# Kernel tuning notes

Measured on AMD Instinct MI355X. Metric: run time of the kernel, lower is better.

## Reference

```python
import jax, jax.numpy as jnp
import numpy as np

DIM = 2048
N_HEADS = 16
HEAD_DIM = DIM // N_HEADS
EPS = 1e-6


def setup_inputs() -> dict:
    key = jax.random.key(0)
    k1, k2, k3, k4, k5 = jax.random.split(key, 5)
    B, S = 2, 2048
    x = jax.random.normal(k1, (B, S, DIM), dtype=jnp.float32)
    cos = jax.random.uniform(k2, (S, HEAD_DIM), dtype=jnp.float32)
    sin = jax.random.uniform(k3, (S, HEAD_DIM), dtype=jnp.float32)
    # torch nn.Linear convention: weight [out_features, in_features], y = x @ W.T
    W_qkv = jax.random.normal(k4, (3 * DIM, DIM), dtype=jnp.float32) * 0.02
    W_proj = jax.random.normal(k5, (DIM, DIM), dtype=jnp.float32) * 0.02
    return {"x": x, "cos": cos, "sin": sin, "W_qkv": W_qkv, "W_proj": W_proj}


def _apply_rope(x, cos, sin):
    # x: [B,H,S,D], cos/sin: [S,D]; rotate interleaved even/odd pairs
    x1, x2 = x[..., ::2], x[..., 1::2]
    c = cos[:, ::2][None, None]  # [1,1,S,D/2]
    s = sin[:, ::2][None, None]
    y1 = x1 * c - x2 * s
    y2 = x1 * s + x2 * c
    return jnp.stack([y1, y2], axis=-1).reshape(x.shape)


def _rms_norm(x):
    # per-head RMS normalization over last dim, no learned scale
    return x * jax.lax.rsqrt(jnp.mean(x * x, axis=-1, keepdims=True) + EPS)


def reference(x, cos, sin, W_qkv, W_proj):
    b, s, d = x.shape
    qkv = jnp.einsum('bsd,ed->bse', x, W_qkv)  # [B,S,3*dim]
    q, k, v = jnp.split(qkv, 3, axis=-1)
    # [B,S,dim] -> [B,H,S,Dh]
    def to_heads(t):
        return t.reshape(b, s, N_HEADS, HEAD_DIM).transpose(0, 2, 1, 3)
    q, k, v = to_heads(q), to_heads(k), to_heads(v)
    q = _apply_rope(_rms_norm(q), cos, sin)
    k = _apply_rope(_rms_norm(k), cos, sin)
    scale = 1.0 / jnp.sqrt(jnp.asarray(HEAD_DIM, dtype=x.dtype))
    scores = jnp.einsum('bhqd,bhkd->bhqk', q, k) * scale  # [B,H,S,S]
    attn = jax.nn.softmax(scores, axis=-1)
    out = jnp.einsum('bhqk,bhkd->bhqd', attn, v)  # [B,H,S,Dh]
    out = out.transpose(0, 2, 1, 3).reshape(b, s, d)
    return jnp.einsum('bsd,od->bso', out, W_proj)
```

## Files before the change

### kernel.cpp

```cpp
#include <hip/hip_runtime.h>
#include <math.h>

#define BATCH 2
#define SEQ   2048
#define DIM   2048
#define NH    16
#define HD    128
#define EPS   1e-6f

typedef _Float16 f16x8 __attribute__((ext_vector_type(8)));
typedef _Float16 f16x4 __attribute__((ext_vector_type(4)));
typedef _Float16 f16x2 __attribute__((ext_vector_type(2)));
typedef float    f32x4 __attribute__((ext_vector_type(4)));

#define MFMA_F16 __builtin_amdgcn_mfma_f32_16x16x32_f16

__global__ __launch_bounds__(256) void cvt_f16(
    const float* __restrict__ in, _Float16* __restrict__ out) {
  int i = blockIdx.x * 256 + threadIdx.x;
  float4 v = ((const float4*)in)[i];
  f16x4 o;
  o[0] = (_Float16)v.x; o[1] = (_Float16)v.y;
  o[2] = (_Float16)v.z; o[3] = (_Float16)v.w;
  ((f16x4*)out)[i] = o;
}

#define BM8 256
#define BN8 128

__global__ __launch_bounds__(512, 2) void gemm_1p(
    const _Float16* __restrict__ Ag, const _Float16* __restrict__ Bg,
    float* __restrict__ C, int M, int N, int K) {
  __shared__ __align__(16) _Float16 smem[2][384][64];

  const int t = threadIdx.x;
  const int w = t >> 6, lane = t & 63;
  const int bm = blockIdx.y * BM8, bn = blockIdx.x * BN8;
  const int wr = (w >> 2) * 128;
  const int wc = (w & 3) * 32;
  const int quad = lane >> 4, c15 = lane & 15;

  const _Float16* baseA = Ag + (size_t)bm * K;
  const _Float16* baseB = Bg + (size_t)bn * K;

  const int lrow = lane >> 3;
  const int lswz = ((lane & 7) ^ lrow) * 8;

  const int col0 = (((0 * 4) + quad) ^ (c15 & 7)) * 8;
  const int col1 = (((1 * 4) + quad) ^ (c15 & 7)) * 8;

  f32x4 acc[8][2] = {};
  f16x8 a0[8], a1[8], b0[2], b1[2];

#define STAGE_TILE(buf, kofs)                                                  \
  {                                                                            \
    _Pragma("unroll")                                                          \
    for (int e = 0; e < 6; ++e) {                                              \
      int c = w * 6 + e;                                                       \
      int rl = c * 8 + lrow;                                                   \
      const _Float16* g = (rl < 256) ? (baseA + (size_t)rl * K)                \
                                     : (baseB + (size_t)(rl - 256) * K);       \
      __builtin_amdgcn_global_load_lds(                                        \
          (const __attribute__((address_space(1))) unsigned int*)(g + (kofs) + lswz), \
          (__attribute__((address_space(3))) unsigned int*)(&smem[buf][c * 8][0]),    \
          16, 0, 0);                                                           \
    }                                                                          \
  }

#define LDA8(dst, colv, buf)                                                   \
  _Pragma("unroll")                                                            \
  for (int m2 = 0; m2 < 8; ++m2)                                               \
    dst[m2] = *(const f16x8*)(&smem[buf][wr + m2 * 16 + c15][colv]);

#define LDB2(dst, colv, buf)                                                   \
  _Pragma("unroll")                                                            \
  for (int n2 = 0; n2 < 2; ++n2)                                               \
    dst[n2] = *(const f16x8*)(&smem[buf][256 + wc + n2 * 16 + c15][colv]);

#define MF16(af, bf)                                                           \
  _Pragma("unroll")                                                            \
  for (int m2 = 0; m2 < 8; ++m2)                                               \
    _Pragma("unroll")                                                          \
    for (int n2 = 0; n2 < 2; ++n2)                                             \
      acc[m2][n2] = MFMA_F16(af[m2], bf[n2], acc[m2][n2], 0, 0, 0);

#define SB() __builtin_amdgcn_sched_barrier(0);

  STAGE_TILE(0, 0)

  const int NT = K >> 6;
  for (int tt = 0; tt < NT; ++tt) {
    const int buf = tt & 1;
    asm volatile("s_waitcnt vmcnt(0)" ::: "memory");
    SB();
    __builtin_amdgcn_s_barrier();
    SB();
    if (tt + 1 < NT) { STAGE_TILE(1 - buf, (tt + 1) * 64) }
    SB();

    LDA8(a0, col0, buf);
    LDB2(b0, col0, buf);
    LDA8(a1, col1, buf);
    LDB2(b1, col1, buf);
    SB();

    __builtin_amdgcn_s_setprio(1);
    MF16(a0, b0);
    __builtin_amdgcn_s_setprio(0);
    SB();
    __builtin_amdgcn_s_setprio(1);
    MF16(a1, b1);
    __builtin_amdgcn_s_setprio(0);
  }

  #pragma unroll
  for (int m2 = 0; m2 < 8; ++m2)
    #pragma unroll
    for (int n2 = 0; n2 < 2; ++n2) {
      int col = bn + wc + 16 * n2 + c15;
      #pragma unroll
      for (int r = 0; r < 4; ++r) {
        int row = bm + wr + 16 * m2 + quad * 4 + r;
        C[(size_t)row * N + col] = acc[m2][n2][r];
      }
    }
#undef STAGE_TILE
#undef LDA8
#undef LDB2
#undef MF16
#undef SB
}

__global__ __launch_bounds__(256) void rmsrope_f16(
    const float* __restrict__ qkv, const float* __restrict__ cosb,
    const float* __restrict__ sinb, _Float16* __restrict__ Qg,
    _Float16* __restrict__ Kg) {
  const int blk = blockIdx.x;
  const int b = blk >> 11, s = blk & (SEQ - 1);
  const int wave = threadIdx.x >> 6, lane = threadIdx.x & 63;
  const float* base = qkv + (size_t)blk * (3 * DIM);
  const float c  = cosb[s * HD + 2 * lane];
  const float sn = sinb[s * HD + 2 * lane];
  #pragma unroll
  for (int h = wave; h < NH; h += 4) {
    float2 q = *(const float2*)(base + h * HD + 2 * lane);
    float2 k = *(const float2*)(base + DIM + h * HD + 2 * lane);
    float ssq = q.x * q.x + q.y * q.y;
    float ssk = k.x * k.x + k.y * k.y;
    #pragma unroll
    for (int off = 32; off >= 1; off >>= 1) {
      ssq += __shfl_xor(ssq, off, 64);
      ssk += __shfl_xor(ssk, off, 64);
    }
    float rq = rsqrtf(ssq * (1.0f / HD) + EPS);
    float rk = rsqrtf(ssk * (1.0f / HD) + EPS);
    float q1 = q.x * rq, q2 = q.y * rq;
    float k1 = k.x * rk, k2 = k.y * rk;
    float qy1 = q1 * c - q2 * sn, qy2 = q1 * sn + q2 * c;
    float ky1 = k1 * c - k2 * sn, ky2 = k1 * sn + k2 * c;
    size_t o = ((size_t)(b * NH + h) * SEQ + s) * HD + 2 * lane;
    f16x2 qo, ko;
    qo[0] = (_Float16)qy1; qo[1] = (_Float16)qy2;
    ko[0] = (_Float16)ky1; ko[1] = (_Float16)ky2;
    *(f16x2*)(Qg + o) = qo;
    *(f16x2*)(Kg + o) = ko;
  }
}

__global__ __launch_bounds__(256) void vtrans_f16(
    const float* __restrict__ qkv, _Float16* __restrict__ Vt) {
  __shared__ _Float16 L[64 * 132];
  const int t = threadIdx.x;
  const int s0 = blockIdx.x * 64, h = blockIdx.y, b = blockIdx.z;
  const float* src = qkv + ((size_t)(b * SEQ + s0)) * (3 * DIM) + 2 * DIM + h * HD;
  #pragma unroll
  for (int it = 0; it < 8; ++it) {
    int f = t + it * 256;
    int r = f >> 5, c4 = f & 31;
    float4 v = *(const float4*)(src + (size_t)r * (3 * DIM) + c4 * 4);
    f16x4 o;
    o[0] = (_Float16)v.x; o[1] = (_Float16)v.y;
    o[2] = (_Float16)v.z; o[3] = (_Float16)v.w;
    *(f16x4*)(&L[r * 132 + c4 * 4]) = o;
  }
  __syncthreads();
  const int d = t >> 1, sc = (t & 1) * 32;
  size_t dst = ((size_t)((b * NH + h) * HD + d)) * SEQ + s0 + sc;
  #pragma unroll
  for (int j = 0; j < 8; ++j) {
    f16x4 o;
    o[0] = L[(sc + 4 * j + 0) * 132 + d];
    o[1] = L[(sc + 4 * j + 1) * 132 + d];
    o[2] = L[(sc + 4 * j + 2) * 132 + d];
    o[3] = L[(sc + 4 * j + 3) * 132 + d];
    *(f16x4*)(Vt + dst + j * 4) = o;
  }
}

#define QT 128
#define KC 32

__global__ __launch_bounds__(256, 2) void flash_f16(
    const _Float16* __restrict__ Qg, const _Float16* __restrict__ Kg,
    const _Float16* __restrict__ Vtg, _Float16* __restrict__ Og) {
  __shared__ __align__(16) _Float16 sm[21504];

  const int t = threadIdx.x, w = t >> 6, lane = t & 63;
  const int quad = lane >> 4, c15 = lane & 15;
  const int bid = blockIdx.x;
  const int grp = (bid & 7) * 4 + ((bid >> 3) >> 4);
  const int qi  = (bid >> 3) & 15;
  const int bh = grp;
  const int hy = grp & (NH - 1), bz = grp >> 4;
  const int q0 = qi * QT;
  const int wr = w * 32;

  {
    const _Float16* qsrc = Qg + ((size_t)bh * SEQ + q0) * HD;
    #pragma unroll
    for (int p = 0; p < 8; ++p) {
      int ci = p * 256 + t;
      int r = ci >> 4, c8 = (ci & 15) ^ (r & 15);
      __builtin_amdgcn_global_load_lds(
          (const __attribute__((address_space(1))) unsigned int*)(qsrc + (size_t)r * HD + c8 * 8),
          (__attribute__((address_space(3))) unsigned int*)(sm + ci * 8), 16, 0, 0);
    }
  }
  __syncthreads();
  f16x8 qf[2][4];
  #pragma unroll
  for (int mf = 0; mf < 2; ++mf)
    #pragma unroll
    for (int ks = 0; ks < 4; ++ks) {
      int m = wr + mf * 16 + c15;
      int c8 = ks * 4 + quad;
      qf[mf][ks] = *(const f16x8*)(sm + (m * 16 + (c8 ^ (m & 15))) * 8);
    }
  asm volatile("s_waitcnt lgkmcnt(0)" ::: "memory");
  __builtin_amdgcn_sched_barrier(0);
  __syncthreads();

  float lrow[8];
  f32x4 oacc[2][8];
  #pragma unroll
  for (int i = 0; i < 8; ++i) lrow[i] = 0.f;
  #pragma unroll
  for (int mf = 0; mf < 2; ++mf)
    #pragma unroll
    for (int nf = 0; nf < 8; ++nf) oacc[mf][nf] = (f32x4){0.f, 0.f, 0.f, 0.f};

  const float sl = 0.12751744f;
  const float M2 = 16.322231f;
  _Float16* Pw = sm + 16384 + w * 1280;

#define STAGE_KV(buf, kk)                                                     \
  _Pragma("unroll")                                                           \
  for (int e = 0; e < 4; ++e) {                                               \
    int idx = w * 4 + e;                                                      \
    int tile = idx >> 3, p = idx & 7;                                         \
    int ci = p * 64 + lane;                                                   \
    if (tile == 0) {                                                          \
      int r = ci >> 4, c8 = (ci & 15) ^ (r & 15);                             \
      int rp = 2 * (r & 15) + (r >> 4);                                       \
      const _Float16* src = Kg +                                              \
          ((size_t)bh * SEQ + (kk) + rp) * HD + c8 * 8;                       \
      __builtin_amdgcn_global_load_lds(                                       \
          (const __attribute__((address_space(1))) unsigned int*)src,         \
          (__attribute__((address_space(3))) unsigned int*)                   \
              (sm + (buf) * 4096 + ci * 8), 16, 0, 0);                        \
    } else {                                                                  \
      int d = ci >> 2, c8 = (ci & 3) ^ (d & 3);                               \
      const _Float16* src = Vtg + (size_t)bh * HD * SEQ + (size_t)d * SEQ     \
          + (kk) + c8 * 8;                                                    \
      __builtin_amdgcn_global_load_lds(                                       \
          (const __attribute__((address_space(1))) unsigned int*)src,         \
          (__attribute__((address_space(3))) unsigned int*)                   \
              (sm + 8192 + (buf) * 4096 + ci * 8), 16, 0, 0);                 \
    }                                                                         \
  }

  STAGE_KV(0, 0)

  const int NC = SEQ / KC;
  for (int it = 0; it < NC; ++it) {
    const int cur = it & 1, cb0 = cur * 4096;
    asm volatile("s_waitcnt vmcnt(0)" ::: "memory");
    __builtin_amdgcn_sched_barrier(0);
    __builtin_amdgcn_s_barrier();
    __builtin_amdgcn_sched_barrier(0);
    if (it + 1 < NC) { STAGE_KV(1 - cur, (it + 1) * KC) }

    f32x4 accs[2][2] = {};
    #pragma unroll
    for (int nf = 0; nf < 2; ++nf) {
      f16x8 kh[4];
      #pragma unroll
      for (int ks = 0; ks < 4; ++ks) {
        int n = nf * 16 + c15;
        int c8 = ks * 4 + quad;
        kh[ks] = *(const f16x8*)(sm + cb0 + (n * 16 + (c8 ^ (n & 15))) * 8);
      }
      __builtin_amdgcn_s_setprio(1);
      #pragma unroll
      for (int ks = 0; ks < 4; ++ks) {
        accs[0][nf] = MFMA_F16(qf[0][ks], kh[ks], accs[0][nf], 0, 0, 0);
        accs[1][nf] = MFMA_F16(qf[1][ks], kh[ks], accs[1][nf], 0, 0, 0);
      }
      __builtin_amdgcn_s_setprio(0);
    }

    #pragma unroll
    for (int mf = 0; mf < 2; ++mf)
      #pragma unroll
      for (int reg = 0; reg < 4; ++reg) {
        float p0 = exp2f(fmaf(accs[mf][0][reg], sl, -M2));
        float p1 = exp2f(fmaf(accs[mf][1][reg], sl, -M2));
        lrow[mf * 4 + reg] += p0 + p1;
        int prow = mf * 16 + quad * 4 + reg;
        f16x2 pp;
        pp[0] = (_Float16)p0; pp[1] = (_Float16)p1;
        *(f16x2*)(Pw + prow * 40 + 2 * c15) = pp;
      }

    f16x8 pa0 = *(const f16x8*)(Pw + (c15) * 40 + quad * 8);
    f16x8 pa1 = *(const f16x8*)(Pw + (16 + c15) * 40 + quad * 8);
    __builtin_amdgcn_s_setprio(1);
    #pragma unroll
    for (int nf = 0; nf < 8; ++nf) {
      int dd = nf * 16 + c15;
      int slot = (dd * 4 + (quad ^ (dd & 3))) * 8;
      f16x8 vv = *(const f16x8*)(sm + 8192 + cb0 + slot);
      oacc[0][nf] = MFMA_F16(pa0, vv, oacc[0][nf], 0, 0, 0);
      oacc[1][nf] = MFMA_F16(pa1, vv, oacc[1][nf], 0, 0, 0);
    }
    __builtin_amdgcn_s_setprio(0);
  }

  #pragma unroll
  for (int i = 0; i < 8; ++i) {
    float s = lrow[i];
    #pragma unroll
    for (int off = 8; off >= 1; off >>= 1) s += __shfl_xor(s, off, 64);
    lrow[i] = s;
  }
  #pragma unroll
  for (int mf = 0; mf < 2; ++mf)
    #pragma unroll
    for (int reg = 0; reg < 4; ++reg) {
      float inv = 1.0f / lrow[mf * 4 + reg];
      int row = q0 + wr + mf * 16 + quad * 4 + reg;
      size_t ob = ((size_t)bz * SEQ + row) * DIM + hy * HD + c15;
      #pragma unroll
      for (int nf = 0; nf < 8; ++nf)
        Og[ob + nf * 16] = (_Float16)(oacc[mf][nf][reg] * inv);
    }
#undef STAGE_KV
}

extern "C" void kernel_launch(void* const* d_in, const int* in_sizes, int n_in,
                              void* d_out, int out_size, void* d_ws, size_t ws_size,
                              hipStream_t stream) {
  const float* x     = (const float*)d_in[0];
  const float* cosb  = (const float*)d_in[1];
  const float* sinb  = (const float*)d_in[2];
  const float* Wqkv  = (const float*)d_in[3];
  const float* Wproj = (const float*)d_in[4];
  float* out = (float*)d_out;

  char* ws = (char*)d_ws;
  float* qkv = (float*)ws;
  char* R = ws + 100663296;
  _Float16* x16 = (_Float16*)(R);
  _Float16* Wh  = (_Float16*)(R + 16777216);
  _Float16* Q16 = (_Float16*)(R);
  _Float16* K16 = (_Float16*)(R + 16777216);
  _Float16* Vt  = (_Float16*)(R + 50331648);
  _Float16* O16 = (_Float16*)(ws);
  _Float16* Wph = (_Float16*)(ws + 16777216);

  cvt_f16<<<8192,  256, 0, stream>>>(x, x16);
  cvt_f16<<<12288, 256, 0, stream>>>(Wqkv, Wh);
  gemm_1p<<<dim3(48, 16), 512, 0, stream>>>(x16, Wh, qkv, 4096, 6144, 2048);
  rmsrope_f16<<<4096, 256, 0, stream>>>(qkv, cosb, sinb, Q16, K16);
  vtrans_f16<<<dim3(32, NH, BATCH), 256, 0, stream>>>(qkv, Vt);
  cvt_f16<<<4096, 256, 0, stream>>>(Wproj, Wph);
  flash_f16<<<512, 256, 0, stream>>>(Q16, K16, Vt, O16);
  gemm_1p<<<dim3(16, 16), 512, 0, stream>>>(O16, Wph, out, 4096, 2048, 2048);
}
```

Baseline: 423.1 us.

## Reshape GEMM tile to 128x256 and software-pipeline LDS reads with MFMA

The GEMM block tile changes from 256x128 to 128x256, and each wave now computes a square 64x64 sub-tile (4x4 MFMA fragments) instead of 128x32. The main loop is restructured so the fragment reads for the second k-half overlap the MFMAs of the first half, and the next tile's first-half reads are issued right after the barrier. Global prefetch now runs two tiles ahead. The aim is better operand reuse per LDS read and hiding LDS latency behind MFMA work. The risk is that the in-flight reuse of LDS buffers is racy or that higher register pressure hurts occupancy.

```diff
diff --git a/kernel.cpp b/kernel.cpp
--- a/kernel.cpp
+++ b/kernel.cpp
@@ -25,9 +25,6 @@
   ((f16x4*)out)[i] = o;
 }
 
-#define BM8 256
-#define BN8 128
-
 __global__ __launch_bounds__(512, 2) void gemm_1p(
     const _Float16* __restrict__ Ag, const _Float16* __restrict__ Bg,
     float* __restrict__ C, int M, int N, int K) {
@@ -35,9 +32,9 @@
 
   const int t = threadIdx.x;
   const int w = t >> 6, lane = t & 63;
-  const int bm = blockIdx.y * BM8, bn = blockIdx.x * BN8;
-  const int wr = (w >> 2) * 128;
-  const int wc = (w & 3) * 32;
+  const int bm = blockIdx.y * 128, bn = blockIdx.x * 256;
+  const int wr = (w >> 2) * 64;
+  const int wc = (w & 3) * 64;
   const int quad = lane >> 4, c15 = lane & 15;
 
   const _Float16* baseA = Ag + (size_t)bm * K;
@@ -46,11 +43,11 @@
   const int lrow = lane >> 3;
   const int lswz = ((lane & 7) ^ lrow) * 8;
 
-  const int col0 = (((0 * 4) + quad) ^ (c15 & 7)) * 8;
-  const int col1 = (((1 * 4) + quad) ^ (c15 & 7)) * 8;
-
-  f32x4 acc[8][2] = {};
-  f16x8 a0[8], a1[8], b0[2], b1[2];
+  const int col0 = ((0 + quad) ^ (c15 & 7)) * 8;
+  const int col1 = ((4 + quad) ^ (c15 & 7)) * 8;
+
+  f32x4 acc[4][4] = {};
+  f16x8 a0[4], b0[4], a1[4], b1[4];
 
 #define STAGE_TILE(buf, kofs)                                                  \
   {                                                                            \
@@ -58,8 +55,8 @@
     for (int e = 0; e < 6; ++e) {                                              \
       int c = w * 6 + e;                                                       \
       int rl = c * 8 + lrow;                                                   \
-      const _Float16* g = (rl < 256) ? (baseA + (size_t)rl * K)                \
-                                     : (baseB + (size_t)(rl - 256) * K);       \
+      const _Float16* g = (rl < 128) ? (baseA + (size_t)rl * K)                \
+                                     : (baseB + (size_t)(rl - 128) * K);       \
       __builtin_amdgcn_global_load_lds(                                        \
           (const __attribute__((address_space(1))) unsigned int*)(g + (kofs) + lswz), \
           (__attribute__((address_space(3))) unsigned int*)(&smem[buf][c * 8][0]),    \
@@ -67,56 +64,54 @@
     }                                                                          \
   }
 
-#define LDA8(dst, colv, buf)                                                   \
+#define RD(dstA, dstB, colv, buf)                                              \
   _Pragma("unroll")                                                            \
-  for (int m2 = 0; m2 < 8; ++m2)                                               \
-    dst[m2] = *(const f16x8*)(&smem[buf][wr + m2 * 16 + c15][colv]);
-
-#define LDB2(dst, colv, buf)                                                   \
+  for (int m2 = 0; m2 < 4; ++m2)                                               \
+    dstA[m2] = *(const f16x8*)(&smem[buf][wr + m2 * 16 + c15][colv]);          \
   _Pragma("unroll")                                                            \
-  for (int n2 = 0; n2 < 2; ++n2)                                               \
-    dst[n2] = *(const f16x8*)(&smem[buf][256 + wc + n2 * 16 + c15][colv]);
-
-#define MF16(af, bf)                                                           \
+  for (int n2 = 0; n2 < 4; ++n2)                                               \
+    dstB[n2] = *(const f16x8*)(&smem[buf][128 + wc + n2 * 16 + c15][colv]);
+
+#define MM(af, bf)                                                             \
   _Pragma("unroll")                                                            \
-  for (int m2 = 0; m2 < 8; ++m2)                                               \
+  for (int m2 = 0; m2 < 4; ++m2)                                               \
     _Pragma("unroll")                                                          \
-    for (int n2 = 0; n2 < 2; ++n2)                                             \
+    for (int n2 = 0; n2 < 4; ++n2)                                             \
       acc[m2][n2] = MFMA_F16(af[m2], bf[n2], acc[m2][n2], 0, 0, 0);
 
 #define SB() __builtin_amdgcn_sched_barrier(0);
 
   STAGE_TILE(0, 0)
+  asm volatile("s_waitcnt vmcnt(0)" ::: "memory");
+  SB();
+  __builtin_amdgcn_s_barrier();
+  SB();
+  STAGE_TILE(1, 64)
+  RD(a0, b0, col0, 0);
 
   const int NT = K >> 6;
   for (int tt = 0; tt < NT; ++tt) {
     const int buf = tt & 1;
+    RD(a1, b1, col1, buf);
+    __builtin_amdgcn_s_setprio(1);
+    MM(a0, b0);
+    __builtin_amdgcn_s_setprio(0);
+    asm volatile("s_waitcnt lgkmcnt(0)" ::: "memory");
     asm volatile("s_waitcnt vmcnt(0)" ::: "memory");
     SB();
     __builtin_amdgcn_s_barrier();
     SB();
-    if (tt + 1 < NT) { STAGE_TILE(1 - buf, (tt + 1) * 64) }
-    SB();
-
-    LDA8(a0, col0, buf);
-    LDB2(b0, col0, buf);
-    LDA8(a1, col1, buf);
-    LDB2(b1, col1, buf);
-    SB();
-
+    if (tt + 2 < NT) { STAGE_TILE(buf, (tt + 2) * 64) }
+    if (tt + 1 < NT) { RD(a0, b0, col0, 1 - buf); }
     __builtin_amdgcn_s_setprio(1);
-    MF16(a0, b0);
+    MM(a1, b1);
     __builtin_amdgcn_s_setprio(0);
-    SB();
-    __builtin_amdgcn_s_setprio(1);
-    MF16(a1, b1);
-    __builtin_amdgcn_s_setprio(0);
-  }
-
-  #pragma unroll
-  for (int m2 = 0; m2 < 8; ++m2)
-    #pragma unroll
-    for (int n2 = 0; n2 < 2; ++n2) {
+  }
+
+  #pragma unroll
+  for (int m2 = 0; m2 < 4; ++m2)
+    #pragma unroll
+    for (int n2 = 0; n2 < 4; ++n2) {
       int col = bn + wc + 16 * n2 + c15;
       #pragma unroll
       for (int r = 0; r < 4; ++r) {
@@ -125,9 +120,8 @@
       }
     }
 #undef STAGE_TILE
-#undef LDA8
-#undef LDB2
-#undef MF16
+#undef RD
+#undef MM
 #undef SB
 }
 
@@ -380,10 +374,10 @@
 
   cvt_f16<<<8192,  256, 0, stream>>>(x, x16);
   cvt_f16<<<12288, 256, 0, stream>>>(Wqkv, Wh);
-  gemm_1p<<<dim3(48, 16), 512, 0, stream>>>(x16, Wh, qkv, 4096, 6144, 2048);
+  gemm_1p<<<dim3(24, 32), 512, 0, stream>>>(x16, Wh, qkv, 4096, 6144, 2048);
   rmsrope_f16<<<4096, 256, 0, stream>>>(qkv, cosb, sinb, Q16, K16);
   vtrans_f16<<<dim3(32, NH, BATCH), 256, 0, stream>>>(qkv, Vt);
   cvt_f16<<<4096, 256, 0, stream>>>(Wproj, Wph);
   flash_f16<<<512, 256, 0, stream>>>(Q16, K16, Vt, O16);
-  gemm_1p<<<dim3(16, 16), 512, 0, stream>>>(O16, Wph, out, 4096, 2048, 2048);
-}
+  gemm_1p<<<dim3(8, 32), 512, 0, stream>>>(O16, Wph, out, 4096, 2048, 2048);
+}
```

Result: faster. 414.0 us (-2.1%).
